# Optimization experiments

Hardware: AMD Instinct MI355X
Metric: run time of the kernel (lower is better)

The kernel has to match this reference:

```python
import jax, jax.numpy as jnp
import numpy as np

SIZE_DICT = 1024  # K
DIM_DICT = 256    # D


def setup_inputs() -> dict:
    key = jax.random.key(0)
    k1, k2, k3 = jax.random.split(key, 3)
    z = jax.random.normal(k1, (64, 1024, DIM_DICT), dtype=jnp.float32)
    codebook = jax.random.normal(k2, (SIZE_DICT, DIM_DICT), dtype=jnp.float32)
    codebook_weight = jax.random.normal(k3, (SIZE_DICT,), dtype=jnp.float32)
    return {
        "z_from_encoder": z,
        "codebook": codebook,
        "codebook_weight": codebook_weight,
        "flg_train": 0,
    }


def reference(z_from_encoder, codebook, codebook_weight, flg_train):
    z = z_from_encoder
    z_flat = z.reshape(-1, DIM_DICT)  # [N, D]
    # Pairwise squared distances: ||z||^2 + ||c||^2 - 2 z.c  -> [N, K]
    cost = (
        jnp.sum(z_flat ** 2, axis=1, keepdims=True)
        + jnp.sum(codebook ** 2, axis=1)
        - 2.0 * jnp.matmul(z_flat, codebook.T)
    )
    idx = jnp.argmin(cost, axis=1)  # [N]
    # one-hot scatter + matmul with codebook == gather of codebook rows
    z_q = codebook[idx].reshape(z.shape)
    # straight-through estimator
    z_q = z + jax.lax.stop_gradient(z_q - z)
    # loss is 0.0 in eval (flg_train False)
    loss = jnp.float32(0.0)
    # perplexity from mean one-hot encodings
    n = z_flat.shape[0]
    counts = jnp.zeros((SIZE_DICT,), dtype=jnp.float32).at[idx].add(1.0)
    e_mean = counts / n
    perplexity = jnp.exp(-jnp.sum(e_mean * jnp.log(e_mean + 1e-10)))
    return z_q, loss, perplexity
```

## Files before the change

### kernel.cpp

```cpp
#include <hip/hip_runtime.h>
#include <hip/hip_bf16.h>
#include <stdint.h>


typedef float  v4f __attribute__((ext_vector_type(4)));
typedef _Float16 v8h __attribute__((ext_vector_type(8)));
typedef _Float16 v4h __attribute__((ext_vector_type(4)));

#define N_ROWS 65536
#define N_DICT 1024
#define DIMS   256
#define MARGIN 4e-3f

__device__ __forceinline__ void gl_lds16(const void* g, void* l) {
  __builtin_amdgcn_global_load_lds(
      (const __attribute__((address_space(1))) unsigned int*)g,
      (__attribute__((address_space(3))) unsigned int*)l,
      16, 0, 0);
}

__global__ void k_prep(const float* __restrict__ cb, _Float16* __restrict__ swz_h,
                       _Float16* __restrict__ swz_l, float* __restrict__ cnA,
                       double* __restrict__ cnD,
                       unsigned* __restrict__ hist, unsigned* __restrict__ counters) {
  const int b = blockIdx.x, t = threadIdx.x;
  if (b == 0) {
    for (int i = t; i < N_DICT; i += 256) hist[i] = 0u;
    if (t == 0) { counters[0] = 0u; counters[1] = 0u; }
  }
  const int gid = b * 256 + t;
  const int col = gid >> 6;
  const int k0  = (gid & 63) * 4;
  v4f v = ((const v4f*)cb)[gid];
  v4h h, l;
  #pragma unroll
  for (int j = 0; j < 4; ++j) {
    h[j] = (_Float16)v[j];
    float r = v[j] - (float)h[j];
    l[j] = (_Float16)r;
  }
  const int c = col >> 6, t4 = (col >> 4) & 3, l15 = col & 15;
  const int kk = k0 >> 5, q = (k0 >> 3) & 3, j0 = k0 & 7;
  const size_t off = (size_t)(((c * 8 + kk) * 4 + t4) * 512 + (q * 16 + l15) * 8 + j0);
  *(v4h*)(swz_h + off) = h;
  *(v4h*)(swz_l + off) = l;
  const int lane = t & 63, w = t >> 6;
  const int row = b * 4 + w;
  v4f u = ((const v4f*)cb)[row * 64 + lane];
  double s = (double)u[0]*u[0] + (double)u[1]*u[1]
           + (double)u[2]*u[2] + (double)u[3]*u[3];
  #pragma unroll
  for (int d = 1; d < 64; d <<= 1) s += __shfl_xor(s, d);
  if (lane == 0) { cnA[row] = (float)s; cnD[row] = s; }
}

__launch_bounds__(512, 2)
__global__ void k_main(const float* __restrict__ z, const _Float16* __restrict__ swz_h,
                       const _Float16* __restrict__ swz_l, const float* __restrict__ cnA,
                       unsigned* __restrict__ out_idx,
                       unsigned long long* __restrict__ list1,
                       unsigned* __restrict__ list2,
                       unsigned* __restrict__ counters) {
  __shared__ __align__(16) char lds[2][65536];
  const int t = threadIdx.x, lane = t & 63, w = t >> 6;
  const int l15 = lane & 15, q = lane >> 4;
  const int waverow = (blockIdx.x * 8 + w) * 32;

  v8h ah[2][8], al[2][8];
  #pragma unroll
  for (int m = 0; m < 2; ++m) {
    const float* zp = z + (size_t)(waverow + m * 16 + l15) * DIMS + q * 8;
    #pragma unroll
    for (int kk = 0; kk < 8; ++kk) {
      v4f f0 = *(const v4f*)(zp + kk * 32);
      v4f f1 = *(const v4f*)(zp + kk * 32 + 4);
      v8h hh, ll;
      #pragma unroll
      for (int j = 0; j < 4; ++j) {
        hh[j] = (_Float16)f0[j];
        float r = f0[j] - (float)hh[j];
        ll[j] = (_Float16)r;
        hh[4 + j] = (_Float16)f1[j];
        r = f1[j] - (float)hh[4 + j];
        ll[4 + j] = (_Float16)r;
      }
      ah[m][kk] = hh; al[m][kk] = ll;
    }
  }

  const int s0 = w * 8;
  const char* gsrc_base = (const char*)(s0 >= 32 ? swz_l : swz_h);
  const int sb = s0 & 31;

  {
    const char* gb = gsrc_base + (size_t)(0 * 32 + sb) * 1024 + lane * 16;
    #pragma unroll
    for (int i = 0; i < 8; ++i)
      gl_lds16(gb + i * 1024, &lds[0][(s0 + i) * 1024]);
  }
  __syncthreads();

  float m1[8], m2[8], m3[8]; int c1[8], c2[8];
  #pragma unroll
  for (int s = 0; s < 8; ++s) {
    m1[s] = 1e30f; m2[s] = 1e30f; m3[s] = 1e30f; c1[s] = 0; c2[s] = 0;
  }

  for (int c = 0; c < 16; ++c) {
    const char* buf = lds[c & 1];
    if (c + 1 < 16) {
      char* nbuf = lds[(c + 1) & 1];
      const char* gb = gsrc_base + (size_t)((c + 1) * 32 + sb) * 1024 + lane * 16;
      #pragma unroll
      for (int i = 0; i < 8; ++i)
        gl_lds16(gb + i * 1024, nbuf + (s0 + i) * 1024);
    }

    const int n0 = c * 64;
    float cn[4]; int colv[4];
    #pragma unroll
    for (int t4 = 0; t4 < 4; ++t4) {
      colv[t4] = n0 + t4 * 16 + l15;
      cn[t4] = cnA[colv[t4]];
    }
    v4f acc[2][4];
    #pragma unroll
    for (int m = 0; m < 2; ++m)
      #pragma unroll
      for (int t4 = 0; t4 < 4; ++t4) acc[m][t4] = (v4f){0.f, 0.f, 0.f, 0.f};

    #pragma unroll
    for (int kk = 0; kk < 8; ++kk) {
      v8h b_h[4], b_l[4];
      #pragma unroll
      for (int t4 = 0; t4 < 4; ++t4)
        b_h[t4] = *(const v8h*)(buf + (kk * 4 + t4) * 1024 + lane * 16);
      #pragma unroll
      for (int t4 = 0; t4 < 4; ++t4)
        b_l[t4] = *(const v8h*)(buf + 32768 + (kk * 4 + t4) * 1024 + lane * 16);
      #pragma unroll
      for (int m = 0; m < 2; ++m) {
        #pragma unroll
        for (int t4 = 0; t4 < 4; ++t4)
          acc[m][t4] = __builtin_amdgcn_mfma_f32_16x16x32_f16(ah[m][kk], b_h[t4], acc[m][t4], 0, 0, 0);
        #pragma unroll
        for (int t4 = 0; t4 < 4; ++t4)
          acc[m][t4] = __builtin_amdgcn_mfma_f32_16x16x32_f16(al[m][kk], b_h[t4], acc[m][t4], 0, 0, 0);
        #pragma unroll
        for (int t4 = 0; t4 < 4; ++t4)
          acc[m][t4] = __builtin_amdgcn_mfma_f32_16x16x32_f16(ah[m][kk], b_l[t4], acc[m][t4], 0, 0, 0);
      }
    }
    #pragma unroll
    for (int m = 0; m < 2; ++m)
      #pragma unroll
      for (int t4 = 0; t4 < 4; ++t4)
        #pragma unroll
        for (int r = 0; r < 4; ++r) {
          float cost = fmaf(acc[m][t4][r], -2.0f, cn[t4]);
          const int s = m * 4 + r;
          bool lt1 = cost < m1[s];
          bool lt2 = cost < m2[s];
          bool lt3 = cost < m3[s];
          m3[s] = lt2 ? m2[s] : (lt3 ? cost : m3[s]);
          m2[s] = lt1 ? m1[s] : (lt2 ? cost : m2[s]);
          c2[s] = lt1 ? c1[s] : (lt2 ? colv[t4] : c2[s]);
          m1[s] = lt1 ? cost : m1[s];
          c1[s] = lt1 ? colv[t4] : c1[s];
        }
    __syncthreads();
  }

  #pragma unroll
  for (int d = 1; d < 16; d <<= 1) {
    #pragma unroll
    for (int s = 0; s < 8; ++s) {
      float om1 = __shfl_xor(m1[s], d);
      float om2 = __shfl_xor(m2[s], d);
      float om3 = __shfl_xor(m3[s], d);
      int   oc1 = __shfl_xor(c1[s], d);
      int   oc2 = __shfl_xor(c2[s], d);
      bool take = (om1 < m1[s]) || (om1 == m1[s] && oc1 < c1[s]);
      float w1 = take ? om1 : m1[s];  int wc1 = take ? oc1 : c1[s];
      float w2 = take ? om2 : m2[s];  int wc2 = take ? oc2 : c2[s];
      float w3 = take ? om3 : m3[s];
      float l1 = take ? m1[s] : om1;  int lc1 = take ? c1[s] : oc1;
      float l2 = take ? m2[s] : om2;
      bool t2 = (l1 < w2) || (l1 == w2 && lc1 < wc2);
      m1[s] = w1; c1[s] = wc1;
      m2[s] = t2 ? l1 : w2;
      c2[s] = t2 ? lc1 : wc2;
      m3[s] = t2 ? fminf(w2, l2) : fminf(w3, l1);
    }
  }
  if (l15 < 8) {
    const int s = l15, m = s >> 2, r = s & 3;
    const int row = waverow + m * 16 + q * 4 + r;
    out_idx[row] = (unsigned)c1[s];
    if (m3[s] - m1[s] < MARGIN) {
      unsigned pos = atomicAdd(&counters[1], 1u);
      list2[pos] = (unsigned)row;
    } else if (m2[s] - m1[s] < MARGIN) {
      unsigned pos = atomicAdd(&counters[0], 1u);
      list1[pos] = (unsigned long long)row
                 | ((unsigned long long)(unsigned)c1[s] << 20)
                 | ((unsigned long long)(unsigned)c2[s] << 40);
    }
  }
}

__global__ void k_pair(const float* __restrict__ z, const float* __restrict__ cb,
                       const double* __restrict__ cnD,
                       const unsigned long long* __restrict__ list1,
                       const unsigned* __restrict__ counters,
                       unsigned* __restrict__ out_idx) {
  const unsigned count = counters[0];
  if (count == 0) return;
  const int t = threadIdx.x, lane = t & 63, w = t >> 6;
  const unsigned gw = blockIdx.x * 4 + w;
  const int half = lane >> 5, l5 = lane & 31;
  for (unsigned g = gw; g < count; g += 1024) {
    const unsigned long long e = list1[g];
    const unsigned row = (unsigned)(e & 0xFFFFFu);
    const int c1 = (int)((e >> 20) & 0x3FFu);
    const int c2 = (int)((e >> 40) & 0x3FFu);
    const int col = half ? c2 : c1;
    const float* cp = cb + (size_t)col * DIMS + l5 * 8;
    const float* zr = z + (size_t)row * DIMS + l5 * 8;
    v4f z0 = *(const v4f*)zr,      z1 = *(const v4f*)(zr + 4);
    v4f cc0 = *(const v4f*)cp,     cc1 = *(const v4f*)(cp + 4);
    double a = (double)z0[0] * (double)cc0[0];
    a = fma((double)z0[1], (double)cc0[1], a);
    a = fma((double)z0[2], (double)cc0[2], a);
    a = fma((double)z0[3], (double)cc0[3], a);
    a = fma((double)z1[0], (double)cc1[0], a);
    a = fma((double)z1[1], (double)cc1[1], a);
    a = fma((double)z1[2], (double)cc1[2], a);
    a = fma((double)z1[3], (double)cc1[3], a);
    #pragma unroll
    for (int d = 1; d < 32; d <<= 1) a += __shfl_xor(a, d);
    double cost = cnD[col] - 2.0 * a;
    double oc = __shfl_xor(cost, 32);
    if (lane == 0) {
      bool take = (oc < cost) || (oc == cost && c2 < c1);
      out_idx[row] = take ? (unsigned)c2 : (unsigned)c1;
    }
  }
}

__global__ void k_deep(const float* __restrict__ z, const float* __restrict__ cb,
                       const double* __restrict__ cnD,
                       const unsigned* __restrict__ list2,
                       const unsigned* __restrict__ counters,
                       unsigned* __restrict__ out_idx) {
  const unsigned count = counters[1];
  if (count == 0) return;
  const int t = threadIdx.x, lane = t & 63, w = t >> 6;
  __shared__ double sc[4];
  __shared__ int scc[4];
  for (unsigned g = blockIdx.x; g < count; g += 256) {
    const unsigned row = list2[g];
    const float* zr = z + (size_t)row * DIMS;
    double best = 1e300; int bc = 1 << 30;
    for (int ci = w * 4; ci < w * 4 + 4; ++ci) {
      const int col = ci * 64 + lane;
      const float* cp = cb + (size_t)col * DIMS;
      double a0 = 0, a1 = 0, a2 = 0, a3 = 0;
      #pragma unroll 4
      for (int k = 0; k < DIMS; k += 4) {
        v4f zz = *(const v4f*)(zr + k);
        v4f cc = *(const v4f*)(cp + k);
        a0 = fma((double)zz[0], (double)cc[0], a0);
        a1 = fma((double)zz[1], (double)cc[1], a1);
        a2 = fma((double)zz[2], (double)cc[2], a2);
        a3 = fma((double)zz[3], (double)cc[3], a3);
      }
      double cost = cnD[col] - 2.0 * ((a0 + a1) + (a2 + a3));
      if (cost < best || (cost == best && col < bc)) { best = cost; bc = col; }
    }
    #pragma unroll
    for (int d = 1; d < 64; d <<= 1) {
      double ob = __shfl_xor(best, d);
      int    oc = __shfl_xor(bc, d);
      if (ob < best || (ob == best && oc < bc)) { best = ob; bc = oc; }
    }
    if (lane == 0) { sc[w] = best; scc[w] = bc; }
    __syncthreads();
    if (t == 0) {
      double b = sc[0]; int c = scc[0];
      #pragma unroll
      for (int i = 1; i < 4; ++i)
        if (sc[i] < b || (sc[i] == b && scc[i] < c)) { b = sc[i]; c = scc[i]; }
      out_idx[row] = (unsigned)c;
    }
    __syncthreads();
  }
}

__global__ void k_gather(const float* __restrict__ cb, const unsigned* __restrict__ idx,
                         float* __restrict__ outz, unsigned* __restrict__ hist) {
  const int t = threadIdx.x, lane = t & 63, w = t >> 6;
  const int base = (blockIdx.x * 4 + w) * 16;
  #pragma unroll 4
  for (int r = 0; r < 16; ++r) {
    const int row = base + r;
    const unsigned id = idx[row];
    v4f v = *(const v4f*)(cb + (size_t)id * DIMS + lane * 4);
    *(v4f*)(outz + (size_t)row * DIMS + lane * 4) = v;
    if (lane == (r & 63)) atomicAdd(hist + id, 1u);
  }
}

__global__ void k_stats(const unsigned* __restrict__ hist, float* __restrict__ out) {
  const int t = threadIdx.x;
  float s = 0.f;
  for (int i = t; i < N_DICT; i += 256) {
    float p = (float)hist[i] * (1.0f / (float)N_ROWS);
    s += p * logf(p + 1e-10f);
  }
  #pragma unroll
  for (int d = 1; d < 64; d <<= 1) s += __shfl_xor(s, d);
  __shared__ float ls[4];
  if ((t & 63) == 0) ls[t >> 6] = s;
  __syncthreads();
  if (t == 0) {
    float tot = ls[0] + ls[1] + ls[2] + ls[3];
    out[16777216] = 0.0f;
    out[16777217] = expf(-tot);
  }
}

extern "C" void kernel_launch(void* const* d_in, const int* in_sizes, int n_in,
                              void* d_out, int out_size, void* d_ws, size_t ws_size,
                              hipStream_t stream) {
  const float* z  = (const float*)d_in[0];
  const float* cb = (const float*)d_in[1];
  float* out = (float*)d_out;
  char* ws = (char*)d_ws;
  _Float16* swz_h            = (_Float16*)ws;
  _Float16* swz_l            = (_Float16*)(ws + 524288);
  float*    cnA              = (float*)(ws + 1048576);
  double*   cnD              = (double*)(ws + 1052672);
  unsigned* idx              = (unsigned*)(ws + 1060864);
  unsigned long long* list1  = (unsigned long long*)(ws + 1323008);
  unsigned* list2            = (unsigned*)(ws + 1847296);
  unsigned* hist             = (unsigned*)(ws + 2109440);
  unsigned* counters         = (unsigned*)(ws + 2113536);

  k_prep  <<<256,  256, 0, stream>>>(cb, swz_h, swz_l, cnA, cnD, hist, counters);
  k_main  <<<256,  512, 0, stream>>>(z, swz_h, swz_l, cnA, idx, list1, list2, counters);
  k_pair  <<<256,  256, 0, stream>>>(z, cb, cnD, list1, counters, idx);
  k_deep  <<<256,  256, 0, stream>>>(z, cb, cnD, list2, counters, idx);
  k_gather<<<1024, 256, 0, stream>>>(cb, idx, out, hist);
  k_stats <<<1,    256, 0, stream>>>(hist, out);
}
```

Before: 247.6 us.

## Halve k_main LDS tile to allow more resident blocks; widen fallback kernel grids

k_main now stages 32 codebook columns per step instead of 64, which halves its double-buffered LDS footprint to 64 KB and raises the launch bound to 4 blocks per CU. The goal is higher occupancy and better latency hiding, at the cost of twice as many loop iterations and barriers. The k_pair and k_deep refinement kernels get larger grids with grid-stride loops, and k_deep uses 8 independent double accumulators to shorten FMA dependency chains. Because k_main launches only 256 blocks, the higher occupancy bound may have little effect, and the tighter bound may constrain registers.

```diff
diff --git a/kernel.cpp b/kernel.cpp
--- a/kernel.cpp
+++ b/kernel.cpp
@@ -54,14 +54,14 @@
   if (lane == 0) { cnA[row] = (float)s; cnD[row] = s; }
 }
 
-__launch_bounds__(512, 2)
+__launch_bounds__(512, 4)
 __global__ void k_main(const float* __restrict__ z, const _Float16* __restrict__ swz_h,
                        const _Float16* __restrict__ swz_l, const float* __restrict__ cnA,
                        unsigned* __restrict__ out_idx,
                        unsigned long long* __restrict__ list1,
                        unsigned* __restrict__ list2,
                        unsigned* __restrict__ counters) {
-  __shared__ __align__(16) char lds[2][65536];
+  __shared__ __align__(16) char lds[2][32768];
   const int t = threadIdx.x, lane = t & 63, w = t >> 6;
   const int l15 = lane & 15, q = lane >> 4;
   const int waverow = (blockIdx.x * 8 + w) * 32;
@@ -88,17 +88,8 @@
     }
   }
 
-  const int s0 = w * 8;
-  const char* gsrc_base = (const char*)(s0 >= 32 ? swz_l : swz_h);
-  const int sb = s0 & 31;
-
-  {
-    const char* gb = gsrc_base + (size_t)(0 * 32 + sb) * 1024 + lane * 16;
-    #pragma unroll
-    for (int i = 0; i < 8; ++i)
-      gl_lds16(gb + i * 1024, &lds[0][(s0 + i) * 1024]);
-  }
-  __syncthreads();
+  const int s0 = w * 4;
+  const char* gsrc_base = (const char*)(s0 >= 16 ? swz_l : swz_h);
 
   float m1[8], m2[8], m3[8]; int c1[8], c2[8];
   #pragma unroll
@@ -106,67 +97,82 @@
     m1[s] = 1e30f; m2[s] = 1e30f; m3[s] = 1e30f; c1[s] = 0; c2[s] = 0;
   }
 
-  for (int c = 0; c < 16; ++c) {
-    const char* buf = lds[c & 1];
-    if (c + 1 < 16) {
-      char* nbuf = lds[(c + 1) & 1];
-      const char* gb = gsrc_base + (size_t)((c + 1) * 32 + sb) * 1024 + lane * 16;
-      #pragma unroll
-      for (int i = 0; i < 8; ++i)
-        gl_lds16(gb + i * 1024, nbuf + (s0 + i) * 1024);
-    }
-
-    const int n0 = c * 64;
-    float cn[4]; int colv[4];
-    #pragma unroll
-    for (int t4 = 0; t4 < 4; ++t4) {
-      colv[t4] = n0 + t4 * 16 + l15;
-      cn[t4] = cnA[colv[t4]];
-    }
-    v4f acc[2][4];
+  {
+    #pragma unroll
+    for (int i = 0; i < 4; ++i) {
+      const int s = s0 + i, kk = (s >> 1) & 7, u = s & 1;
+      const char* gb = gsrc_base + (size_t)(kk * 4096 + u * 1024 + lane * 16);
+      gl_lds16(gb, &lds[0][s * 1024]);
+    }
+  }
+  __syncthreads();
+
+  for (int cc = 0; cc < 32; ++cc) {
+    const char* buf = lds[cc & 1];
+    if (cc + 1 < 32) {
+      const int nc = cc + 1, c = nc >> 1, half = nc & 1;
+      char* nbuf = lds[nc & 1];
+      #pragma unroll
+      for (int i = 0; i < 4; ++i) {
+        const int s = s0 + i, kk = (s >> 1) & 7, u = s & 1;
+        const char* gb = gsrc_base +
+            (size_t)(c * 32768 + kk * 4096 + (2 * half + u) * 1024 + lane * 16);
+        gl_lds16(gb, nbuf + s * 1024);
+      }
+    }
+
+    const int c = cc >> 1, half = cc & 1;
+    const int n0 = c * 64 + half * 32;
+    float cn[2]; int colv[2];
+    #pragma unroll
+    for (int u = 0; u < 2; ++u) {
+      colv[u] = n0 + u * 16 + l15;
+      cn[u] = cnA[colv[u]];
+    }
+    v4f acc[2][2];
     #pragma unroll
     for (int m = 0; m < 2; ++m)
       #pragma unroll
-      for (int t4 = 0; t4 < 4; ++t4) acc[m][t4] = (v4f){0.f, 0.f, 0.f, 0.f};
+      for (int u = 0; u < 2; ++u) acc[m][u] = (v4f){0.f, 0.f, 0.f, 0.f};
 
     #pragma unroll
     for (int kk = 0; kk < 8; ++kk) {
-      v8h b_h[4], b_l[4];
-      #pragma unroll
-      for (int t4 = 0; t4 < 4; ++t4)
-        b_h[t4] = *(const v8h*)(buf + (kk * 4 + t4) * 1024 + lane * 16);
-      #pragma unroll
-      for (int t4 = 0; t4 < 4; ++t4)
-        b_l[t4] = *(const v8h*)(buf + 32768 + (kk * 4 + t4) * 1024 + lane * 16);
+      v8h b_h[2], b_l[2];
+      #pragma unroll
+      for (int u = 0; u < 2; ++u)
+        b_h[u] = *(const v8h*)(buf + (kk * 2 + u) * 1024 + lane * 16);
+      #pragma unroll
+      for (int u = 0; u < 2; ++u)
+        b_l[u] = *(const v8h*)(buf + 16384 + (kk * 2 + u) * 1024 + lane * 16);
       #pragma unroll
       for (int m = 0; m < 2; ++m) {
         #pragma unroll
-        for (int t4 = 0; t4 < 4; ++t4)
-          acc[m][t4] = __builtin_amdgcn_mfma_f32_16x16x32_f16(ah[m][kk], b_h[t4], acc[m][t4], 0, 0, 0);
+        for (int u = 0; u < 2; ++u)
+          acc[m][u] = __builtin_amdgcn_mfma_f32_16x16x32_f16(ah[m][kk], b_h[u], acc[m][u], 0, 0, 0);
         #pragma unroll
-        for (int t4 = 0; t4 < 4; ++t4)
-          acc[m][t4] = __builtin_amdgcn_mfma_f32_16x16x32_f16(al[m][kk], b_h[t4], acc[m][t4], 0, 0, 0);
+        for (int u = 0; u < 2; ++u)
+          acc[m][u] = __builtin_amdgcn_mfma_f32_16x16x32_f16(al[m][kk], b_h[u], acc[m][u], 0, 0, 0);
         #pragma unroll
-        for (int t4 = 0; t4 < 4; ++t4)
-          acc[m][t4] = __builtin_amdgcn_mfma_f32_16x16x32_f16(ah[m][kk], b_l[t4], acc[m][t4], 0, 0, 0);
+        for (int u = 0; u < 2; ++u)
+          acc[m][u] = __builtin_amdgcn_mfma_f32_16x16x32_f16(ah[m][kk], b_l[u], acc[m][u], 0, 0, 0);
       }
     }
     #pragma unroll
     for (int m = 0; m < 2; ++m)
       #pragma unroll
-      for (int t4 = 0; t4 < 4; ++t4)
+      for (int u = 0; u < 2; ++u)
         #pragma unroll
         for (int r = 0; r < 4; ++r) {
-          float cost = fmaf(acc[m][t4][r], -2.0f, cn[t4]);
+          float cost = fmaf(acc[m][u][r], -2.0f, cn[u]);
           const int s = m * 4 + r;
           bool lt1 = cost < m1[s];
           bool lt2 = cost < m2[s];
           bool lt3 = cost < m3[s];
           m3[s] = lt2 ? m2[s] : (lt3 ? cost : m3[s]);
           m2[s] = lt1 ? m1[s] : (lt2 ? cost : m2[s]);
-          c2[s] = lt1 ? c1[s] : (lt2 ? colv[t4] : c2[s]);
+          c2[s] = lt1 ? c1[s] : (lt2 ? colv[u] : c2[s]);
           m1[s] = lt1 ? cost : m1[s];
-          c1[s] = lt1 ? colv[t4] : c1[s];
+          c1[s] = lt1 ? colv[u] : c1[s];
         }
     __syncthreads();
   }
@@ -218,8 +224,9 @@
   if (count == 0) return;
   const int t = threadIdx.x, lane = t & 63, w = t >> 6;
   const unsigned gw = blockIdx.x * 4 + w;
+  const unsigned nw = gridDim.x * 4;
   const int half = lane >> 5, l5 = lane & 31;
-  for (unsigned g = gw; g < count; g += 1024) {
+  for (unsigned g = gw; g < count; g += nw) {
     const unsigned long long e = list1[g];
     const unsigned row = (unsigned)(e & 0xFFFFFu);
     const int c1 = (int)((e >> 20) & 0x3FFu);
@@ -258,24 +265,31 @@
   const int t = threadIdx.x, lane = t & 63, w = t >> 6;
   __shared__ double sc[4];
   __shared__ int scc[4];
-  for (unsigned g = blockIdx.x; g < count; g += 256) {
+  for (unsigned g = blockIdx.x; g < count; g += gridDim.x) {
     const unsigned row = list2[g];
     const float* zr = z + (size_t)row * DIMS;
     double best = 1e300; int bc = 1 << 30;
     for (int ci = w * 4; ci < w * 4 + 4; ++ci) {
       const int col = ci * 64 + lane;
       const float* cp = cb + (size_t)col * DIMS;
-      double a0 = 0, a1 = 0, a2 = 0, a3 = 0;
-      #pragma unroll 4
-      for (int k = 0; k < DIMS; k += 4) {
-        v4f zz = *(const v4f*)(zr + k);
-        v4f cc = *(const v4f*)(cp + k);
-        a0 = fma((double)zz[0], (double)cc[0], a0);
-        a1 = fma((double)zz[1], (double)cc[1], a1);
-        a2 = fma((double)zz[2], (double)cc[2], a2);
-        a3 = fma((double)zz[3], (double)cc[3], a3);
+      double a0 = 0, a1 = 0, a2 = 0, a3 = 0, a4 = 0, a5 = 0, a6 = 0, a7 = 0;
+      #pragma unroll 8
+      for (int k = 0; k < DIMS; k += 8) {
+        v4f z0 = *(const v4f*)(zr + k);
+        v4f z1 = *(const v4f*)(zr + k + 4);
+        v4f cc0 = *(const v4f*)(cp + k);
+        v4f cc1 = *(const v4f*)(cp + k + 4);
+        a0 = fma((double)z0[0], (double)cc0[0], a0);
+        a1 = fma((double)z0[1], (double)cc0[1], a1);
+        a2 = fma((double)z0[2], (double)cc0[2], a2);
+        a3 = fma((double)z0[3], (double)cc0[3], a3);
+        a4 = fma((double)z1[0], (double)cc1[0], a4);
+        a5 = fma((double)z1[1], (double)cc1[1], a5);
+        a6 = fma((double)z1[2], (double)cc1[2], a6);
+        a7 = fma((double)z1[3], (double)cc1[3], a7);
       }
-      double cost = cnD[col] - 2.0 * ((a0 + a1) + (a2 + a3));
+      double cost = cnD[col]
+                  - 2.0 * (((a0 + a1) + (a2 + a3)) + ((a4 + a5) + (a6 + a7)));
       if (cost < best || (cost == best && col < bc)) { best = cost; bc = col; }
     }
     #pragma unroll
@@ -349,8 +363,8 @@
 
   k_prep  <<<256,  256, 0, stream>>>(cb, swz_h, swz_l, cnA, cnD, hist, counters);
   k_main  <<<256,  512, 0, stream>>>(z, swz_h, swz_l, cnA, idx, list1, list2, counters);
-  k_pair  <<<256,  256, 0, stream>>>(z, cb, cnD, list1, counters, idx);
-  k_deep  <<<256,  256, 0, stream>>>(z, cb, cnD, list2, counters, idx);
+  k_pair  <<<1024, 256, 0, stream>>>(z, cb, cnD, list1, counters, idx);
+  k_deep  <<<2048, 256, 0, stream>>>(z, cb, cnD, list2, counters, idx);
   k_gather<<<1024, 256, 0, stream>>>(cb, idx, out, hist);
   k_stats <<<1,    256, 0, stream>>>(hist, out);
 }
```

New measurement: 428.1 us. +72.9%, slower.
